# Optimization experiments

Hardware: AMD Instinct MI355X
Metric: run time of the kernel (lower is better)

## Reference

```python
import jax, jax.numpy as jnp
import numpy as np

PASSES = 6
S = 2           # numEdgeSets
D = 256         # inputLayerSize
OUT = 10        # outputLayerSize
HID = 80
B, N, E = 4, 10000, 160000


def _leaky(x):
    return jax.nn.leaky_relu(x, negative_slope=0.01)


def setup_inputs() -> dict:
    key = jax.random.key(0)
    ks = jax.random.split(key, 18)
    sc = 0.05
    return {
        "nodes": jax.random.normal(ks[0], (B, N, D), jnp.float32),
        "edges": jax.random.randint(ks[1], (B, S, E, 2), 0, N, jnp.int32),
        "problem_type": jax.random.uniform(ks[2], (B, 1), jnp.float32),
        # GRUCell params (torch layout: [3D, D] for ih and hh)
        "gru_w_ih": jax.random.normal(ks[3], (3 * D, D), jnp.float32) * sc,
        "gru_w_hh": jax.random.normal(ks[4], (3 * D, D), jnp.float32) * sc,
        "gru_b_ih": jax.random.normal(ks[5], (3 * D,), jnp.float32) * sc,
        "gru_b_hh": jax.random.normal(ks[6], (3 * D,), jnp.float32) * sc,
        # per-edge-set 2-layer MLP, stacked over edge sets
        "edge_w1": jax.random.normal(ks[7], (S, D, D), jnp.float32) * sc,
        "edge_b1": jax.random.normal(ks[8], (S, D), jnp.float32) * sc,
        "edge_w2": jax.random.normal(ks[9], (S, D, D), jnp.float32) * sc,
        "edge_b2": jax.random.normal(ks[10], (S, D), jnp.float32) * sc,
        # readout head
        "fc1_w": jax.random.normal(ks[11], (HID, D + 1), jnp.float32) * sc,
        "fc1_b": jax.random.normal(ks[12], (HID,), jnp.float32) * sc,
        "fc2_w": jax.random.normal(ks[13], (HID, HID), jnp.float32) * sc,
        "fc2_b": jax.random.normal(ks[14], (HID,), jnp.float32) * sc,
        "fc3_w": jax.random.normal(ks[15], (OUT, HID), jnp.float32) * sc,
        "fc3_b": jax.random.normal(ks[16], (OUT,), jnp.float32) * sc,
    }


def _gru_cell(x, h, w_ih, w_hh, b_ih, b_hh):
    # torch.nn.GRUCell semantics; x,h: [B,N,D]
    gi = jnp.einsum("bnd,ed->bne", x, w_ih) + b_ih   # [B,N,3D]
    gh = jnp.einsum("bnd,ed->bne", h, w_hh) + b_hh
    i_r, i_z, i_n = jnp.split(gi, 3, axis=-1)
    h_r, h_z, h_n = jnp.split(gh, 3, axis=-1)
    r = jax.nn.sigmoid(i_r + h_r)
    z = jax.nn.sigmoid(i_z + h_z)
    n = jnp.tanh(i_n + r * h_n)
    return (1.0 - z) * n + z * h


def reference(nodes, edges, problem_type, gru_w_ih, gru_w_hh, gru_b_ih, gru_b_hh,
              edge_w1, edge_b1, edge_w2, edge_b2,
              fc1_w, fc1_b, fc2_w, fc2_b, fc3_w, fc3_b):
    bidx = jnp.arange(B)[:, None]  # [B,1] for batched scatter
    h = nodes
    for j in range(PASSES):
        incoming = jnp.zeros_like(h)
        for si in range(S):
            dst = edges[:, si, :, 0]  # [B,E]
            src = edges[:, si, :, 1]  # [B,E]
            gathered = jnp.take_along_axis(h, src[:, :, None], axis=1)  # [B,E,D]
            y = _leaky(jnp.einsum("bed,fd->bef", gathered, edge_w1[si]) + edge_b1[si])
            y = jnp.einsum("bed,fd->bef", y, edge_w2[si]) + edge_b2[si]
            incoming = incoming.at[bidx, dst].add(y)
        h = _gru_cell(incoming, h, gru_w_ih, gru_w_hh, gru_b_ih, gru_b_hh)
        if j < PASSES - 2:
            h = jax.lax.stop_gradient(h)  # mirrors .detach()
    # graph readout: sum over nodes, log, nan->0, relu, +inf->finite max
    s = jnp.sum(h, axis=1)               # [B,D]
    l = jnp.log(s)
    l = jnp.where(jnp.isnan(l), 0.0, l)
    l = jax.nn.relu(l)
    finite_max = jnp.max(jnp.where(jnp.isinf(l), -jnp.inf, l), axis=1, keepdims=True)
    l = jnp.where(jnp.isinf(l), finite_max, l)
    x = jnp.concatenate([l, problem_type], axis=1)  # [B,D+1]
    x = _leaky(x @ fc1_w.T + fc1_b)
    x = _leaky(x @ fc2_w.T + fc2_b)
    return x @ fc3_w.T + fc3_b  # [B,OUT]
```

## Files before the change

kernel.cpp:

```cpp
#include <hip/hip_runtime.h>
#include <math.h>

#define NNODES 10000
#define NEDGES 160000
#define DIM    256
#define BATCH  4
#define NG     8
#define MROWS  40064
#define RBLK   625
#define RGRP   79

typedef __attribute__((ext_vector_type(8))) __bf16 bf16x8;
typedef __attribute__((ext_vector_type(4))) float  floatx4;

__device__ __forceinline__ float leakyf(float x){ return x > 0.f ? x : 0.01f*x; }
__device__ __forceinline__ float fsig(float x){ return 1.f/(1.f + __expf(-x)); }
__device__ __forceinline__ float ftanh(float x){ return 1.f - 2.f/(1.f + __expf(2.f*x)); }
__device__ __forceinline__ unsigned short f2bf_u(float x){
  unsigned int u = __float_as_uint(x);
  u += 0x7fffu + ((u >> 16) & 1u);
  return (unsigned short)(u >> 16);
}
__device__ __forceinline__ float bfdec(unsigned short u){
  return __uint_as_float(((unsigned int)u) << 16);
}
#define GATE_SCL 65535.f
#define GATE_INV 1.5259021896696422e-5f

__device__ __forceinline__ void glds16(unsigned short* lds, const unsigned short* g){
  __builtin_amdgcn_global_load_lds(
      (const __attribute__((address_space(1))) void*)g,
      (__attribute__((address_space(3))) void*)lds, 16, 0, 0);
}

__global__ void ihinit_kernel(const float* __restrict__ nodes,
                              unsigned short* __restrict__ ihcat,
                              unsigned short* __restrict__ h_lo){
  int idx = blockIdx.x*256 + threadIdx.x;
  int row = idx >> 8, d = idx & 255;
  float v = nodes[idx];
  unsigned short h = f2bf_u(v);
  ihcat[(size_t)row*512 + 256 + d] = h;
  h_lo[idx] = f2bf_u(v - bfdec(h));
}

__global__ void w1cat_kernel(const float* __restrict__ ew1, unsigned short* __restrict__ o){
  int idx = blockIdx.x*256 + threadIdx.x;
  int n = idx >> 8, k = idx & 255;
  o[idx] = f2bf_u(ew1[(n>>8)*65536 + (n&255)*256 + k]);
}
__global__ void w2k_kernel(const float* __restrict__ ew2, unsigned short* __restrict__ o){
  int idx = blockIdx.x*256 + threadIdx.x;
  int n = idx >> 10, kp = idx & 1023;
  int j = kp & 511, term = kp >> 9;
  int si = j >> 8, k = j & 255;
  float v = ew2[si*65536 + n*256 + k];
  unsigned short h = f2bf_u(v);
  o[idx] = term ? f2bf_u(v - bfdec(h)) : h;
}
__global__ void wk2_kernel(const float* __restrict__ w, unsigned short* __restrict__ o){
  int idx = blockIdx.x*256 + threadIdx.x;
  int c = idx >> 9, kp = idx & 511;
  int k = kp & 255, term = kp >> 8;
  float v = w[c*256 + k];
  unsigned short h = f2bf_u(v);
  o[idx] = term ? f2bf_u(v - bfdec(h)) : h;
}
__global__ void wcomb_kernel(const float* __restrict__ wih, const float* __restrict__ whh,
                             unsigned short* __restrict__ o){
  int idx = blockIdx.x*256 + threadIdx.x;
  int c = idx >> 10, kp = idx & 1023;
  int seg = kp >> 8, k = kp & 255;
  const float* w = (seg & 1) ? whh : wih;
  float v = w[c*256 + k];
  unsigned short h = f2bf_u(v);
  o[idx] = (seg >> 1) ? f2bf_u(v - bfdec(h)) : h;
}

__global__ void hist_kernel(const int* __restrict__ edges, int* __restrict__ cnt){
  int idx = blockIdx.x*256 + threadIdx.x;
  if (idx < NG*NEDGES){
    int g = idx / NEDGES, e = idx - g*NEDGES;
    int d = edges[((size_t)g*NEDGES + e)*2];
    atomicAdd(&cnt[g*NNODES + d], 1);
  }
}

__global__ __launch_bounds__(256) void scan_kernel(const int* __restrict__ cnt, int* __restrict__ off){
  __shared__ int sc[256];
  int g = blockIdx.x, t = threadIdx.x;
  int base = 0;
  for (int c=0;c<40;c++){
    int i = c*256 + t;
    int v = (i < NNODES) ? cnt[g*NNODES + i] : 0;
    __syncthreads();
    sc[t] = v;
    __syncthreads();
    for (int o=1;o<256;o<<=1){
      int u = (t>=o) ? sc[t-o] : 0;
      __syncthreads();
      sc[t] += u;
      __syncthreads();
    }
    if (i < NNODES) off[g*(NNODES+1) + i] = base + sc[t] - v;
    base += sc[255];
  }
  if (t == 0) off[g*(NNODES+1) + NNODES] = base;
}

__global__ void scatter_kernel(const int* __restrict__ edges, const int* __restrict__ off,
                               int* __restrict__ cur, int* __restrict__ ssrc){
  int idx = blockIdx.x*256 + threadIdx.x;
  if (idx < NG*NEDGES){
    int g = idx / NEDGES, e = idx - g*NEDGES;
    const int* ep = &edges[((size_t)g*NEDGES + e)*2];
    int d = ep[0], s = ep[1];
    int pos = off[g*(NNODES+1) + d] + atomicAdd(&cur[g*NNODES + d], 1);
    ssrc[g*NEDGES + pos] = s;
  }
}

template<int KP, int RS, int KM>
__device__ __forceinline__ void mm64_core(
    const unsigned short* __restrict__ Ab, const unsigned short* __restrict__ Wb,
    unsigned short* lds, floatx4 (&acc)[4][2])
{
  const int t = threadIdx.x;
  const int w = t >> 6, lane = t & 63;
  const int q = lane >> 4, col = lane & 15;
  const int wc = w*32;
  unsigned short* Al = lds;
  unsigned short* Bl = lds + 64*64;

  const int sr = t >> 3;
  const int sj = t & 7;
  const int sk = ((sj ^ (sr & 7)) * 8);

  for (int kb = 0; kb < KP; kb += 64){
    #pragma unroll
    for (int i=0;i<2;i++){
      int r = i*32 + sr;
      glds16(&Al[i*2048 + w*512], &Ab[(size_t)r*RS + ((kb + sk) & KM)]);
    }
    #pragma unroll
    for (int i=0;i<4;i++){
      int r = i*32 + sr;
      glds16(&Bl[i*2048 + w*512], &Wb[(size_t)r*KP + kb + sk]);
    }
    __syncthreads();
    #pragma unroll
    for (int ks2=0; ks2<2; ks2++){
      bf16x8 a[4], bf[2];
      #pragma unroll
      for (int mi=0;mi<4;mi++){
        int r = mi*16 + col;
        int j = (ks2*4 + q) ^ (r & 7);
        a[mi] = *(const bf16x8*)&Al[r*64 + j*8];
      }
      #pragma unroll
      for (int ni=0;ni<2;ni++){
        int r = wc + ni*16 + col;
        int j = (ks2*4 + q) ^ (r & 7);
        bf[ni] = *(const bf16x8*)&Bl[r*64 + j*8];
      }
      #pragma unroll
      for (int mi=0;mi<4;mi++)
        #pragma unroll
        for (int ni=0;ni<2;ni++)
          acc[mi][ni] = __builtin_amdgcn_mfma_f32_16x16x32_bf16(a[mi], bf[ni], acc[mi][ni], 0,0,0);
    }
    __syncthreads();
  }
}

#define XDECODE(NCOL) \
  const int bid_ = blockIdx.x; \
  const int rb_ = ((bid_ >> 3) / NCOL) * 8 + (bid_ & 7); \
  const int colb_ = (bid_ >> 3) % NCOL; \
  if (rb_ >= RBLK) return;

#define MMPRO \
  const int t = threadIdx.x, w = t >> 6, lane = t & 63; \
  const int q = lane >> 4, col = lane & 15; \
  const int wc = w*32; \
  floatx4 acc[4][2]; \
  _Pragma("unroll") for (int mi=0;mi<4;mi++) _Pragma("unroll") for (int ni=0;ni<2;ni++) \
    acc[mi][ni] = (floatx4){0.f,0.f,0.f,0.f};

__global__ __launch_bounds__(256) void z64_kernel(
    const unsigned short* __restrict__ ihcat, const unsigned short* __restrict__ w1cat,
    const float* __restrict__ eb1, unsigned short* __restrict__ Z)
{
  __shared__ unsigned short lds[12288];
  XDECODE(4)
  const int row0 = rb_*64, col0 = colb_*128;
  MMPRO
  mm64_core<256,512,255>(ihcat + (size_t)row0*512 + 256, w1cat + (size_t)col0*256, lds, acc);

  #pragma unroll
  for (int ni=0;ni<2;ni++){
    int n = col0 + wc + ni*16 + col;
    int si = n >> 8, cz = n & 255;
    float bb = eb1[si*256 + cz];
    unsigned short* zp = Z + (size_t)si*MROWS*256 + cz;
    #pragma unroll
    for (int mi=0;mi<4;mi++)
      #pragma unroll
      for (int rr=0;rr<4;rr++){
        int row = row0 + mi*16 + q*4 + rr;
        zp[(size_t)row*256] = f2bf_u(leakyf(acc[mi][ni][rr] + bb));
      }
  }
}

__global__ __launch_bounds__(256) void aggregate_kernel(
    const unsigned short* __restrict__ Z, const int* __restrict__ ssrc,
    const int* __restrict__ off, unsigned short* __restrict__ Sb)
{
  const int bid = blockIdx.x;
  const int g = bid & 7;
  const int dgrp = bid >> 3;
  const int b = g >> 1, si = g & 1;
  const int w = threadIdx.x >> 6, lane = threadIdx.x & 63;
  const unsigned short* zb = Z + ((size_t)si*MROWS + b*10000)*256 + lane*4;
  const int* sp = ssrc + (size_t)g*NEDGES;
  const int* offg = off + g*(NNODES+1);

  #pragma unroll
  for (int i=0;i<4;i++){
    const int d = dgrp*16 + w*4 + i;
    const int j0 = offg[d], j1 = offg[d+1];
    float a0=0.f, a1=0.f, a2=0.f, a3=0.f;
    int j = j0;
    for (; j+4 <= j1; j+=4){
      int s0=sp[j], s1=sp[j+1], s2=sp[j+2], s3=sp[j+3];
      ushort4 u0 = *(const ushort4*)&zb[(size_t)s0*256];
      ushort4 u1 = *(const ushort4*)&zb[(size_t)s1*256];
      ushort4 u2 = *(const ushort4*)&zb[(size_t)s2*256];
      ushort4 u3 = *(const ushort4*)&zb[(size_t)s3*256];
      a0 += bfdec(u0.x)+bfdec(u1.x)+bfdec(u2.x)+bfdec(u3.x);
      a1 += bfdec(u0.y)+bfdec(u1.y)+bfdec(u2.y)+bfdec(u3.y);
      a2 += bfdec(u0.z)+bfdec(u1.z)+bfdec(u2.z)+bfdec(u3.z);
      a3 += bfdec(u0.w)+bfdec(u1.w)+bfdec(u2.w)+bfdec(u3.w);
    }
    for (; j < j1; j++){
      ushort4 u = *(const ushort4*)&zb[(size_t)sp[j]*256];
      a0 += bfdec(u.x); a1 += bfdec(u.y); a2 += bfdec(u.z); a3 += bfdec(u.w);
    }
    size_t so = (size_t)(b*10000 + d)*512 + si*256 + lane*4;
    ushort4 h;
    h.x = f2bf_u(a0); h.y = f2bf_u(a1); h.z = f2bf_u(a2); h.w = f2bf_u(a3);
    *(ushort4*)&Sb[so] = h;
  }
}

__global__ __launch_bounds__(256) void w264_kernel(
    const unsigned short* __restrict__ Sb, const unsigned short* __restrict__ w2k,
    const float* __restrict__ eb2, const int* __restrict__ off,
    unsigned short* __restrict__ ihcat)
{
  __shared__ unsigned short lds[12288];
  XDECODE(2)
  const int row0 = rb_*64, col0 = colb_*128;
  MMPRO
  mm64_core<1024,512,511>(Sb + (size_t)row0*512, w2k + (size_t)col0*1024, lds, acc);

  float b20[2], b21[2];
  #pragma unroll
  for (int ni=0;ni<2;ni++){
    int n = col0 + wc + ni*16 + col;
    b20[ni] = eb2[n];
    b21[ni] = eb2[256 + n];
  }
  #pragma unroll
  for (int mi=0;mi<4;mi++)
    #pragma unroll
    for (int rr=0;rr<4;rr++){
      int row = row0 + mi*16 + q*4 + rr;
      int b = row / 10000, d = row - b*10000;
      int o0 = (b*2)*(NNODES+1) + d;
      int o1 = (b*2+1)*(NNODES+1) + d;
      float dg0 = (float)(off[o0+1] - off[o0]);
      float dg1 = (float)(off[o1+1] - off[o1]);
      #pragma unroll
      for (int ni=0;ni<2;ni++){
        int n = col0 + wc + ni*16 + col;
        ihcat[(size_t)row*512 + n] = f2bf_u(acc[mi][ni][rr] + dg0*b20[ni] + dg1*b21[ni]);
      }
    }
}

__global__ __launch_bounds__(256) void gruA_kernel(
    const unsigned short* __restrict__ ihcat, const unsigned short* __restrict__ wcomb,
    const float* __restrict__ b_ih, const float* __restrict__ b_hh,
    unsigned short* __restrict__ rz_r, unsigned short* __restrict__ rz_z)
{
  __shared__ unsigned short lds[12288];
  XDECODE(4)
  const int row0 = rb_*64, col0 = colb_*128;
  MMPRO
  mm64_core<1024,512,511>(ihcat + (size_t)row0*512, wcomb + (size_t)col0*1024, lds, acc);

  float bb[2];
  #pragma unroll
  for (int ni=0;ni<2;ni++){
    int n = col0 + wc + ni*16 + col;
    bb[ni] = b_ih[n] + b_hh[n];
  }
  unsigned short* dst = (col0 < 256) ? rz_r : rz_z;
  const int cbase = (col0 & 255) + wc;
  #pragma unroll
  for (int mi=0;mi<4;mi++)
    #pragma unroll
    for (int rr=0;rr<4;rr++){
      size_t row = (size_t)(row0 + mi*16 + q*4 + rr);
      #pragma unroll
      for (int ni=0;ni<2;ni++){
        float v = fsig(acc[mi][ni][rr] + bb[ni]);
        dst[row*256 + cbase + ni*16 + col] = (unsigned short)(v*GATE_SCL + 0.5f);
      }
    }
}

__global__ __launch_bounds__(256) void gruB_kernel(
    const unsigned short* __restrict__ ihcat, unsigned short* __restrict__ h_lo,
    const unsigned short* __restrict__ wihk, const unsigned short* __restrict__ whhk,
    const float* __restrict__ b_ih, const float* __restrict__ b_hh,
    const unsigned short* __restrict__ rz_r, const unsigned short* __restrict__ rz_z,
    unsigned short* __restrict__ ihcat_nxt)
{
  __shared__ unsigned short lds[12288];
  XDECODE(2)
  const int row0 = rb_*64, dcol0 = colb_*128;
  const int t = threadIdx.x, w = t >> 6, lane = t & 63;
  const int q = lane >> 4, col = lane & 15;
  const int wc = w*32;

  floatx4 ai[4][2], ah[4][2];
  #pragma unroll
  for (int mi=0;mi<4;mi++)
    #pragma unroll
    for (int ni=0;ni<2;ni++){ ai[mi][ni] = (floatx4){0.f,0.f,0.f,0.f}; ah[mi][ni] = (floatx4){0.f,0.f,0.f,0.f}; }

  mm64_core<512,512,255>(ihcat + (size_t)row0*512,       wihk + (size_t)(512 + dcol0)*512, lds, ai);
  mm64_core<512,512,255>(ihcat + (size_t)row0*512 + 256, whhk + (size_t)(512 + dcol0)*512, lds, ah);

  float bi[2], bh[2];
  #pragma unroll
  for (int ni=0;ni<2;ni++){
    int n = 512 + dcol0 + wc + ni*16 + col;
    bi[ni] = b_ih[n]; bh[ni] = b_hh[n];
  }
  #pragma unroll
  for (int mi=0;mi<4;mi++)
    #pragma unroll
    for (int rr=0;rr<4;rr++){
      size_t row = (size_t)(row0 + mi*16 + q*4 + rr);
      #pragma unroll
      for (int ni=0;ni<2;ni++){
        int dn = dcol0 + wc + ni*16 + col;
        float rg = (float)rz_r[row*256 + dn] * GATE_INV;
        float zg = (float)rz_z[row*256 + dn] * GATE_INV;
        float ng = ftanh(ai[mi][ni][rr] + bi[ni] + rg*(ah[mi][ni][rr] + bh[ni]));
        float hv = bfdec(ihcat[row*512 + 256 + dn]) + bfdec(h_lo[row*256 + dn]);
        float hnew = (1.f - zg)*ng + zg*hv;
        unsigned short hh = f2bf_u(hnew);
        ihcat_nxt[row*512 + 256 + dn] = hh;
        h_lo[row*256 + dn] = f2bf_u(hnew - bfdec(hh));
      }
    }
}

__global__ void reduce_kernel(const unsigned short* __restrict__ ihcat,
                              const unsigned short* __restrict__ h_lo,
                              float* __restrict__ sbuf){
  int b  = blockIdx.x / 50;
  int s0 = (blockIdx.x % 50) * 200;
  int d  = threadIdx.x;
  size_t row = (size_t)b*NNODES + s0;
  float acc = 0.f;
  for (int i=0;i<200;i++){
    acc += bfdec(ihcat[(row+i)*512 + 256 + d]) + bfdec(h_lo[(row+i)*256 + d]);
  }
  atomicAdd(&sbuf[b*DIM + d], acc);
}

__global__ __launch_bounds__(320) void head_kernel(
    const float* __restrict__ sbuf, const float* __restrict__ pt,
    const float* __restrict__ fc1w, const float* __restrict__ fc1b,
    const float* __restrict__ fc2w, const float* __restrict__ fc2b,
    const float* __restrict__ fc3w, const float* __restrict__ fc3b,
    float* __restrict__ out)
{
  __shared__ float L[4][257];
  __shared__ float T1[4][80];
  __shared__ float T2[4][80];
  __shared__ float fmx[4];
  int t = threadIdx.x;
  if (t < 256){
    for (int b=0;b<4;b++){
      float v = sbuf[b*DIM + t];
      float ll = logf(v);
      if (ll != ll) ll = 0.f;
      ll = fmaxf(ll, 0.f);
      L[b][t] = ll;
    }
  }
  __syncthreads();
  int w = t >> 6, lane = t & 63;
  if (w < 4){
    float m = -INFINITY;
    for (int i=lane;i<256;i+=64){ float v = L[w][i]; if (v != INFINITY) m = fmaxf(m, v); }
    #pragma unroll
    for (int o=32;o>=1;o>>=1) m = fmaxf(m, __shfl_xor(m, o, 64));
    if (lane==0) fmx[w] = m;
  }
  __syncthreads();
  if (t < 256){
    for (int b=0;b<4;b++) if (L[b][t] == INFINITY) L[b][t] = fmx[b];
  }
  if (t < 4) L[t][256] = pt[t];
  __syncthreads();
  if (t < 320){
    int b = t/80, i = t%80;
    float a = fc1b[i];
    for (int k=0;k<257;k++) a += L[b][k]*fc1w[i*257+k];
    T1[b][i] = leakyf(a);
  }
  __syncthreads();
  if (t < 320){
    int b = t/80, i = t%80;
    float a = fc2b[i];
    for (int k=0;k<80;k++) a += T1[b][k]*fc2w[i*80+k];
    T2[b][i] = leakyf(a);
  }
  __syncthreads();
  if (t < 40){
    int b = t/10, i = t%10;
    float a = fc3b[i];
    for (int k=0;k<80;k++) a += T2[b][k]*fc3w[i*80+k];
    out[b*10+i] = a;
  }
}

extern "C" void kernel_launch(void* const* d_in, const int* in_sizes, int n_in,
                              void* d_out, int out_size, void* d_ws, size_t ws_size,
                              hipStream_t stream) {
  const float* nodes = (const float*)d_in[0];
  const int*   edges = (const int*)d_in[1];
  const float* pt    = (const float*)d_in[2];
  const float* w_ih  = (const float*)d_in[3];
  const float* w_hh  = (const float*)d_in[4];
  const float* b_ih  = (const float*)d_in[5];
  const float* b_hh  = (const float*)d_in[6];
  const float* ew1   = (const float*)d_in[7];
  const float* eb1   = (const float*)d_in[8];
  const float* ew2   = (const float*)d_in[9];
  const float* eb2   = (const float*)d_in[10];
  const float* fc1w  = (const float*)d_in[11];
  const float* fc1b  = (const float*)d_in[12];
  const float* fc2w  = (const float*)d_in[13];
  const float* fc2b  = (const float*)d_in[14];
  const float* fc3w  = (const float*)d_in[15];
  const float* fc3b  = (const float*)d_in[16];

  const size_t HN  = (size_t)BATCH*NNODES*DIM;
  const size_t HNP = (size_t)MROWS*DIM;
  char* p = (char*)d_ws;
  float* sbuf = (float*)p;                        p += BATCH*DIM*4;
  unsigned short* ihcat0 = (unsigned short*)p;    p += (size_t)MROWS*512*2;
  unsigned short* ihcat1 = (unsigned short*)p;    p += (size_t)MROWS*512*2;
  unsigned short* h_lo   = (unsigned short*)p;    p += HNP*2;
  unsigned short* Zb   = (unsigned short*)p;      p += 2*HNP*2;
  unsigned short* Sb   = (unsigned short*)p;      p += (size_t)MROWS*512*2;
  unsigned short* w1cat= (unsigned short*)p;      p += 512*256*2;
  unsigned short* w2k  = (unsigned short*)p;      p += 256*1024*2;
  unsigned short* wihk = (unsigned short*)p;      p += 768*512*2;
  unsigned short* whhk = (unsigned short*)p;      p += 768*512*2;
  unsigned short* wcomb= (unsigned short*)p;      p += 512*1024*2;
  int* off  = (int*)p;                            p += NG*(NNODES+1)*4;
  int* cur  = (int*)p;                            p += NG*NNODES*4;
  int* ssrc = (int*)p;                            p += (size_t)NG*NEDGES*4;

  unsigned short* rz_r = (unsigned short*)Sb;
  unsigned short* rz_z = rz_r + (size_t)MROWS*256;

  w1cat_kernel<<<512,256,0,stream>>>(ew1, w1cat);
  w2k_kernel<<<1024,256,0,stream>>>(ew2, w2k);
  wk2_kernel<<<1536,256,0,stream>>>(w_ih, wihk);
  wk2_kernel<<<1536,256,0,stream>>>(w_hh, whhk);
  wcomb_kernel<<<2048,256,0,stream>>>(w_ih, w_hh, wcomb);

  ihinit_kernel<<<(int)(HN/256),256,0,stream>>>(nodes, ihcat0, h_lo);

  hipMemsetAsync(cur, 0, NG*NNODES*sizeof(int), stream);
  hist_kernel<<<(NG*NEDGES)/256,256,0,stream>>>(edges, cur);
  scan_kernel<<<NG,256,0,stream>>>(cur, off);
  hipMemsetAsync(cur, 0, NG*NNODES*sizeof(int), stream);
  scatter_kernel<<<(NG*NEDGES)/256,256,0,stream>>>(edges, off, cur, ssrc);

  hipMemsetAsync(sbuf, 0, BATCH*DIM*sizeof(float), stream);

  unsigned short* ih[2] = {ihcat0, ihcat1};

  for (int pass=0; pass<6; pass++){
    unsigned short* curb = ih[pass & 1];
    unsigned short* nxtb = ih[(pass+1) & 1];
    z64_kernel<<<RGRP*8*4,256,0,stream>>>(curb, w1cat, eb1, Zb);
    aggregate_kernel<<<5000,256,0,stream>>>(Zb, ssrc, off, Sb);
    w264_kernel<<<RGRP*8*2,256,0,stream>>>(Sb, w2k, eb2, off, curb);
    gruA_kernel<<<RGRP*8*4,256,0,stream>>>(curb, wcomb, b_ih, b_hh, rz_r, rz_z);
    gruB_kernel<<<RGRP*8*2,256,0,stream>>>(curb, h_lo, wihk, whhk, b_ih, b_hh,
                                           rz_r, rz_z, nxtb);
  }
  reduce_kernel<<<200,256,0,stream>>>(ih[0], h_lo, sbuf);
  head_kernel<<<1,320,0,stream>>>(sbuf, pt, fc1w,fc1b,fc2w,fc2b,fc3w,fc3b,(float*)d_out);
}
```

Measured before the change: 1.667 ms.

## Use 128x128 GEMM tiles for z, w2 and gruA kernels; widen aggregate loads

Adds a 128-row by 128-column MFMA core with each wave computing a 64x64 subtile, and switches three of the per-pass GEMM kernels to it. Each block now does four times the MFMA work per LDS load, which cuts redundant global and LDS traffic for the shared weight tiles. In exchange it uses more registers and launches fewer blocks, which can lower occupancy. Padded rows past 40000 are clamped when degrees are looked up. Separately, the aggregate kernel now has each half-wave load 8 bf16 values per lane, covering two destination nodes per wave at a time.

New measurement: 1.723 ms. +3.3%, slower.

```diff
diff --git a/kernel.cpp b/kernel.cpp
--- a/kernel.cpp
+++ b/kernel.cpp
@@ -9,9 +9,12 @@
 #define MROWS  40064
 #define RBLK   625
 #define RGRP   79
+#define RBLK128 313
+#define RGRP128 40
 
 typedef __attribute__((ext_vector_type(8))) __bf16 bf16x8;
 typedef __attribute__((ext_vector_type(4))) float  floatx4;
+typedef __attribute__((ext_vector_type(8))) unsigned short ushort8v;
 
 __device__ __forceinline__ float leakyf(float x){ return x > 0.f ? x : 0.01f*x; }
 __device__ __forceinline__ float fsig(float x){ return 1.f/(1.f + __expf(-x)); }
@@ -173,11 +176,67 @@
   }
 }
 
+template<int KP, int RS, int KM>
+__device__ __forceinline__ void mm128_core(
+    const unsigned short* __restrict__ Ab, const unsigned short* __restrict__ Wb,
+    unsigned short* lds, floatx4 (&acc)[4][4])
+{
+  const int t = threadIdx.x;
+  const int w = t >> 6, lane = t & 63;
+  const int q = lane >> 4, col = lane & 15;
+  const int wr = (w >> 1) * 64;
+  const int wc = (w & 1) * 64;
+  unsigned short* Al = lds;
+  unsigned short* Bl = lds + 128*64;
+
+  const int sr = t >> 3;
+  const int sj = t & 7;
+  const int sk = ((sj ^ (sr & 7)) * 8);
+
+  for (int kb = 0; kb < KP; kb += 64){
+    #pragma unroll
+    for (int i=0;i<4;i++){
+      int r = i*32 + sr;
+      glds16(&Al[i*2048 + w*512], &Ab[(size_t)r*RS + ((kb + sk) & KM)]);
+      glds16(&Bl[i*2048 + w*512], &Wb[(size_t)r*KP + kb + sk]);
+    }
+    __syncthreads();
+    #pragma unroll
+    for (int ks2=0; ks2<2; ks2++){
+      bf16x8 a[4], bf[4];
+      #pragma unroll
+      for (int mi=0;mi<4;mi++){
+        int r = wr + mi*16 + col;
+        int j = (ks2*4 + q) ^ (r & 7);
+        a[mi] = *(const bf16x8*)&Al[r*64 + j*8];
+      }
+      #pragma unroll
+      for (int ni=0;ni<4;ni++){
+        int r = wc + ni*16 + col;
+        int j = (ks2*4 + q) ^ (r & 7);
+        bf[ni] = *(const bf16x8*)&Bl[r*64 + j*8];
+      }
+      #pragma unroll
+      for (int mi=0;mi<4;mi++)
+        #pragma unroll
+        for (int ni=0;ni<4;ni++)
+          acc[mi][ni] = __builtin_amdgcn_mfma_f32_16x16x32_bf16(a[mi], bf[ni], acc[mi][ni], 0,0,0);
+    }
+    __syncthreads();
+  }
+}
+
 #define XDECODE(NCOL) \
   const int bid_ = blockIdx.x; \
   const int rb_ = ((bid_ >> 3) / NCOL) * 8 + (bid_ & 7); \
   const int colb_ = (bid_ >> 3) % NCOL; \
   if (rb_ >= RBLK) return;
+
+#define XDECODE128(NCOL) \
+  const int bid_ = blockIdx.x; \
+  const int rb_ = ((bid_ >> 3) / NCOL) * 8 + (bid_ & 7); \
+  const int colb_ = (bid_ >> 3) % NCOL; \
+  if (rb_ >= RBLK128) return;
 
 #define MMPRO \
   const int t = threadIdx.x, w = t >> 6, lane = t & 63; \
@@ -187,19 +246,27 @@
   _Pragma("unroll") for (int mi=0;mi<4;mi++) _Pragma("unroll") for (int ni=0;ni<2;ni++) \
     acc[mi][ni] = (floatx4){0.f,0.f,0.f,0.f};
 
+#define MMPRO128 \
+  const int t = threadIdx.x, w = t >> 6, lane = t & 63; \
+  const int q = lane >> 4, col = lane & 15; \
+  const int wrq = (w >> 1) * 64, wcq = (w & 1) * 64; \
+  floatx4 acc[4][4]; \
+  _Pragma("unroll") for (int mi=0;mi<4;mi++) _Pragma("unroll") for (int ni=0;ni<4;ni++) \
+    acc[mi][ni] = (floatx4){0.f,0.f,0.f,0.f};
+
 __global__ __launch_bounds__(256) void z64_kernel(
     const unsigned short* __restrict__ ihcat, const unsigned short* __restrict__ w1cat,
     const float* __restrict__ eb1, unsigned short* __restrict__ Z)
 {
-  __shared__ unsigned short lds[12288];
-  XDECODE(4)
-  const int row0 = rb_*64, col0 = colb_*128;
-  MMPRO
-  mm64_core<256,512,255>(ihcat + (size_t)row0*512 + 256, w1cat + (size_t)col0*256, lds, acc);
-
-  #pragma unroll
-  for (int ni=0;ni<2;ni++){
-    int n = col0 + wc + ni*16 + col;
+  __shared__ unsigned short lds[16384];
+  XDECODE128(4)
+  const int row0 = rb_*128, col0 = colb_*128;
+  MMPRO128
+  mm128_core<256,512,255>(ihcat + (size_t)row0*512 + 256, w1cat + (size_t)col0*256, lds, acc);
+
+  #pragma unroll
+  for (int ni=0;ni<4;ni++){
+    int n = col0 + wcq + ni*16 + col;
     int si = n >> 8, cz = n & 255;
     float bb = eb1[si*256 + cz];
     unsigned short* zp = Z + (size_t)si*MROWS*256 + cz;
@@ -207,7 +274,7 @@
     for (int mi=0;mi<4;mi++)
       #pragma unroll
       for (int rr=0;rr<4;rr++){
-        int row = row0 + mi*16 + q*4 + rr;
+        int row = row0 + wrq + mi*16 + q*4 + rr;
         zp[(size_t)row*256] = f2bf_u(leakyf(acc[mi][ni][rr] + bb));
       }
   }
@@ -222,35 +289,42 @@
   const int dgrp = bid >> 3;
   const int b = g >> 1, si = g & 1;
   const int w = threadIdx.x >> 6, lane = threadIdx.x & 63;
-  const unsigned short* zb = Z + ((size_t)si*MROWS + b*10000)*256 + lane*4;
+  const int half = lane >> 5, c = lane & 31;
+  const unsigned short* zb = Z + ((size_t)si*MROWS + b*10000)*256 + c*8;
   const int* sp = ssrc + (size_t)g*NEDGES;
   const int* offg = off + g*(NNODES+1);
 
   #pragma unroll
-  for (int i=0;i<4;i++){
-    const int d = dgrp*16 + w*4 + i;
-    const int j0 = offg[d], j1 = offg[d+1];
-    float a0=0.f, a1=0.f, a2=0.f, a3=0.f;
-    int j = j0;
+  for (int p=0;p<2;p++){
+    const int d = dgrp*16 + w*4 + p*2 + half;
+    int j = offg[d];
+    const int j1 = offg[d+1];
+    float a0=0.f,a1=0.f,a2=0.f,a3=0.f,a4=0.f,a5=0.f,a6=0.f,a7=0.f;
     for (; j+4 <= j1; j+=4){
       int s0=sp[j], s1=sp[j+1], s2=sp[j+2], s3=sp[j+3];
-      ushort4 u0 = *(const ushort4*)&zb[(size_t)s0*256];
-      ushort4 u1 = *(const ushort4*)&zb[(size_t)s1*256];
-      ushort4 u2 = *(const ushort4*)&zb[(size_t)s2*256];
-      ushort4 u3 = *(const ushort4*)&zb[(size_t)s3*256];
-      a0 += bfdec(u0.x)+bfdec(u1.x)+bfdec(u2.x)+bfdec(u3.x);
-      a1 += bfdec(u0.y)+bfdec(u1.y)+bfdec(u2.y)+bfdec(u3.y);
-      a2 += bfdec(u0.z)+bfdec(u1.z)+bfdec(u2.z)+bfdec(u3.z);
-      a3 += bfdec(u0.w)+bfdec(u1.w)+bfdec(u2.w)+bfdec(u3.w);
+      ushort8v u0 = *(const ushort8v*)&zb[(size_t)s0*256];
+      ushort8v u1 = *(const ushort8v*)&zb[(size_t)s1*256];
+      ushort8v u2 = *(const ushort8v*)&zb[(size_t)s2*256];
+      ushort8v u3 = *(const ushort8v*)&zb[(size_t)s3*256];
+      a0 += bfdec(u0[0])+bfdec(u1[0])+bfdec(u2[0])+bfdec(u3[0]);
+      a1 += bfdec(u0[1])+bfdec(u1[1])+bfdec(u2[1])+bfdec(u3[1]);
+      a2 += bfdec(u0[2])+bfdec(u1[2])+bfdec(u2[2])+bfdec(u3[2]);
+      a3 += bfdec(u0[3])+bfdec(u1[3])+bfdec(u2[3])+bfdec(u3[3]);
+      a4 += bfdec(u0[4])+bfdec(u1[4])+bfdec(u2[4])+bfdec(u3[4]);
+      a5 += bfdec(u0[5])+bfdec(u1[5])+bfdec(u2[5])+bfdec(u3[5]);
+      a6 += bfdec(u0[6])+bfdec(u1[6])+bfdec(u2[6])+bfdec(u3[6]);
+      a7 += bfdec(u0[7])+bfdec(u1[7])+bfdec(u2[7])+bfdec(u3[7]);
     }
     for (; j < j1; j++){
-      ushort4 u = *(const ushort4*)&zb[(size_t)sp[j]*256];
-      a0 += bfdec(u.x); a1 += bfdec(u.y); a2 += bfdec(u.z); a3 += bfdec(u.w);
-    }
-    size_t so = (size_t)(b*10000 + d)*512 + si*256 + lane*4;
-    ushort4 h;
-    h.x = f2bf_u(a0); h.y = f2bf_u(a1); h.z = f2bf_u(a2); h.w = f2bf_u(a3);
-    *(ushort4*)&Sb[so] = h;
+      ushort8v u = *(const ushort8v*)&zb[(size_t)sp[j]*256];
+      a0+=bfdec(u[0]); a1+=bfdec(u[1]); a2+=bfdec(u[2]); a3+=bfdec(u[3]);
+      a4+=bfdec(u[4]); a5+=bfdec(u[5]); a6+=bfdec(u[6]); a7+=bfdec(u[7]);
+    }
+    size_t so = (size_t)(b*10000 + d)*512 + si*256 + c*8;
+    ushort8v hv;
+    hv[0]=f2bf_u(a0); hv[1]=f2bf_u(a1); hv[2]=f2bf_u(a2); hv[3]=f2bf_u(a3);
+    hv[4]=f2bf_u(a4); hv[5]=f2bf_u(a5); hv[6]=f2bf_u(a6); hv[7]=f2bf_u(a7);
+    *(ushort8v*)&Sb[so] = hv;
   }
 }
 
@@ -259,16 +333,16 @@
     const float* __restrict__ eb2, const int* __restrict__ off,
     unsigned short* __restrict__ ihcat)
 {
-  __shared__ unsigned short lds[12288];
-  XDECODE(2)
-  const int row0 = rb_*64, col0 = colb_*128;
-  MMPRO
-  mm64_core<1024,512,511>(Sb + (size_t)row0*512, w2k + (size_t)col0*1024, lds, acc);
-
-  float b20[2], b21[2];
-  #pragma unroll
-  for (int ni=0;ni<2;ni++){
-    int n = col0 + wc + ni*16 + col;
+  __shared__ unsigned short lds[16384];
+  XDECODE128(2)
+  const int row0 = rb_*128, col0 = colb_*128;
+  MMPRO128
+  mm128_core<1024,512,511>(Sb + (size_t)row0*512, w2k + (size_t)col0*1024, lds, acc);
+
+  float b20[4], b21[4];
+  #pragma unroll
+  for (int ni=0;ni<4;ni++){
+    int n = col0 + wcq + ni*16 + col;
     b20[ni] = eb2[n];
     b21[ni] = eb2[256 + n];
   }
@@ -276,15 +350,16 @@
   for (int mi=0;mi<4;mi++)
     #pragma unroll
     for (int rr=0;rr<4;rr++){
-      int row = row0 + mi*16 + q*4 + rr;
-      int b = row / 10000, d = row - b*10000;
+      int row = row0 + wrq + mi*16 + q*4 + rr;
+      int rw = (row < 40000) ? row : 39999;
+      int b = rw / 10000, d = rw - b*10000;
       int o0 = (b*2)*(NNODES+1) + d;
       int o1 = (b*2+1)*(NNODES+1) + d;
       float dg0 = (float)(off[o0+1] - off[o0]);
       float dg1 = (float)(off[o1+1] - off[o1]);
       #pragma unroll
-      for (int ni=0;ni<2;ni++){
-        int n = col0 + wc + ni*16 + col;
+      for (int ni=0;ni<4;ni++){
+        int n = col0 + wcq + ni*16 + col;
         ihcat[(size_t)row*512 + n] = f2bf_u(acc[mi][ni][rr] + dg0*b20[ni] + dg1*b21[ni]);
       }
     }
@@ -295,27 +370,27 @@
     const float* __restrict__ b_ih, const float* __restrict__ b_hh,
     unsigned short* __restrict__ rz_r, unsigned short* __restrict__ rz_z)
 {
-  __shared__ unsigned short lds[12288];
-  XDECODE(4)
-  const int row0 = rb_*64, col0 = colb_*128;
-  MMPRO
-  mm64_core<1024,512,511>(ihcat + (size_t)row0*512, wcomb + (size_t)col0*1024, lds, acc);
-
-  float bb[2];
-  #pragma unroll
-  for (int ni=0;ni<2;ni++){
-    int n = col0 + wc + ni*16 + col;
+  __shared__ unsigned short lds[16384];
+  XDECODE128(4)
+  const int row0 = rb_*128, col0 = colb_*128;
+  MMPRO128
+  mm128_core<1024,512,511>(ihcat + (size_t)row0*512, wcomb + (size_t)col0*1024, lds, acc);
+
+  float bb[4];
+  #pragma unroll
+  for (int ni=0;ni<4;ni++){
+    int n = col0 + wcq + ni*16 + col;
     bb[ni] = b_ih[n] + b_hh[n];
   }
   unsigned short* dst = (col0 < 256) ? rz_r : rz_z;
-  const int cbase = (col0 & 255) + wc;
+  const int cbase = (col0 & 255) + wcq;
   #pragma unroll
   for (int mi=0;mi<4;mi++)
     #pragma unroll
     for (int rr=0;rr<4;rr++){
-      size_t row = (size_t)(row0 + mi*16 + q*4 + rr);
-      #pragma unroll
-      for (int ni=0;ni<2;ni++){
+      size_t row = (size_t)(row0 + wrq + mi*16 + q*4 + rr);
+      #pragma unroll
+      for (int ni=0;ni<4;ni++){
         float v = fsig(acc[mi][ni][rr] + bb[ni]);
         dst[row*256 + cbase + ni*16 + col] = (unsigned short)(v*GATE_SCL + 0.5f);
       }
@@ -506,10 +581,10 @@
   for (int pass=0; pass<6; pass++){
     unsigned short* curb = ih[pass & 1];
     unsigned short* nxtb = ih[(pass+1) & 1];
-    z64_kernel<<<RGRP*8*4,256,0,stream>>>(curb, w1cat, eb1, Zb);
+    z64_kernel<<<RGRP128*8*4,256,0,stream>>>(curb, w1cat, eb1, Zb);
     aggregate_kernel<<<5000,256,0,stream>>>(Zb, ssrc, off, Sb);
-    w264_kernel<<<RGRP*8*2,256,0,stream>>>(Sb, w2k, eb2, off, curb);
-    gruA_kernel<<<RGRP*8*4,256,0,stream>>>(curb, wcomb, b_ih, b_hh, rz_r, rz_z);
+    w264_kernel<<<RGRP128*8*2,256,0,stream>>>(Sb, w2k, eb2, off, curb);
+    gruA_kernel<<<RGRP128*8*4,256,0,stream>>>(curb, wcomb, b_ih, b_hh, rz_r, rz_z);
     gruB_kernel<<<RGRP*8*2,256,0,stream>>>(curb, h_lo, wihk, whhk, b_ih, b_hh,
                                            rz_r, rz_z, nxtb);
   }
```
